# Kernel tuning notes

Measured on AMD Instinct MI355X. Metric: run time of the kernel, lower is better.

## Reference

```python
import jax, jax.numpy as jnp
from jax import lax
import numpy as np


def _conv(x, w):
    # x: [B,Cin,H,W], w: [Cout,Cin,kh,kw] -> [B,Cout,H,W], SAME padding
    return lax.conv_general_dilated(x, w, (1, 1), 'SAME')


def setup_inputs() -> dict:
    key = jax.random.key(0)
    ks = jax.random.split(key, 16)
    B, Hh, W = 8, 256, 256
    inputs = jax.random.normal(ks[0], (B, Hh, W), jnp.float32)
    H0 = jax.random.normal(ks[1], (B, Hh, W), jnp.float32)
    C0 = jax.random.normal(ks[2], (B, 2, Hh, W), jnp.float32)
    # learned scalars: c2 ~ U(0,1), sf ~ N(0, 0.01) shifted away from 0 (it is a divisor)
    c2 = jax.random.uniform(ks[3], (1,), jnp.float32, 0.0, 1.0)
    sf = 0.01 * jax.random.normal(ks[4], (1,), jnp.float32) + 0.02
    # RedNet (assumed small conv encoder-decoder): 1->32->64->32->1, 3x3 SAME, ReLU
    w1 = 0.1 * jax.random.normal(ks[5], (32, 1, 3, 3), jnp.float32)
    b1 = jnp.zeros((32,), jnp.float32)
    w2 = 0.1 * jax.random.normal(ks[6], (64, 32, 3, 3), jnp.float32)
    b2 = jnp.zeros((64,), jnp.float32)
    w3 = 0.1 * jax.random.normal(ks[7], (32, 64, 3, 3), jnp.float32)
    b3 = jnp.zeros((32,), jnp.float32)
    w4 = 0.1 * jax.random.normal(ks[8], (1, 32, 3, 3), jnp.float32)
    b4 = jnp.zeros((1,), jnp.float32)
    return dict(inputs=inputs, H0=H0, C0=C0, c2=c2, sf=sf,
                w1=w1, b1=b1, w2=w2, b2=b2, w3=w3, b3=b3, w4=w4, b4=b4)


def reference(inputs, H0, C0, c2, sf, w1, b1, w2, b2, w3, b3, w4, b4):
    # Fixed 5-point Laplacian stencil (non-trainable in the original module)
    lap_k = jnp.array([[0., 1., 0.], [1., -4., 1.], [0., 1., 0.]],
                      dtype=inputs.dtype)[None, None]  # [1,1,3,3]

    # torch chain: C' = permute/matmul(Wcc^T)/permute + wcu*U
    #   reduces exactly to: C'[:,0] = inputs, C'[:,1] = C_old[:,0]
    C_new = jnp.stack([inputs, C0[:, 0]], axis=1)  # [B,2,H,W]

    V = inputs - H0  # [B,H,W]

    # H = whc . C' = 2*C'[:,0] - C'[:,1] = 2*inputs - C_old[:,0]
    lap = _conv(inputs[:, None], lap_k)[:, 0]  # [B,H,W]
    H = 2.0 * inputs - C0[:, 0] + c2 * lap

    # RedNet on scaled residual V
    h = (V / sf)[:, None]  # [B,1,H,W]
    h = jax.nn.relu(_conv(h, w1) + b1[None, :, None, None])
    h = jax.nn.relu(_conv(h, w2) + b2[None, :, None, None])
    h = jax.nn.relu(_conv(h, w3) + b3[None, :, None, None])
    V_hat = (_conv(h, w4) + b4[None, :, None, None])[:, 0] * sf  # [B,H,W]

    outputs = H + V_hat
    return (outputs, H, C_new, V, V_hat)
```

## Files before the change

### kernel.cpp

```cpp
#include <hip/hip_runtime.h>

#define PLANE 65536
#define WIDTH 256
#define PADW 258
#define PADPLANE 66564

typedef __bf16 v8bf __attribute__((ext_vector_type(8)));
typedef float  v4f  __attribute__((ext_vector_type(4)));

typedef const __attribute__((address_space(1))) unsigned int* gas_ptr;
typedef __attribute__((address_space(3))) unsigned int* las_ptr;

__device__ __forceinline__ void gl_lds(const void* g, void* l) {
  __builtin_amdgcn_global_load_lds((gas_ptr)g, (las_ptr)l, 16, 0, 0);
}

__device__ __forceinline__ int swz(int c) {
  return (c & ~7) | ((c & 7) ^ ((c >> 3) & 7));
}

__device__ __forceinline__ int m6(int x) { return x >= 6 ? x - 6 : x; }

__device__ __forceinline__ unsigned int pack2(float a, float b) {
  __bf16 ba = (__bf16)a, bb = (__bf16)b;
  unsigned short sa = __builtin_bit_cast(unsigned short, ba);
  unsigned short sb = __builtin_bit_cast(unsigned short, bb);
  return (unsigned int)sa | ((unsigned int)sb << 16);
}

#define WT_N 37440
#define ZR_N (8 * 1028 * 32)
__global__ __launch_bounds__(256) void wz_k(
    const float* __restrict__ w1, const float* __restrict__ w2,
    const float* __restrict__ w3, const float* __restrict__ w4,
    float* __restrict__ w1t, __bf16* __restrict__ B2t,
    __bf16* __restrict__ B3t, float* __restrict__ w4t,
    __bf16* __restrict__ a1, __bf16* __restrict__ a3)
{
  int t = blockIdx.x * 256 + threadIdx.x;
  if (t < WT_N) {
    if (t < 288) {
      int tap = t >> 5, cout = t & 31;
      w1t[t] = w1[cout * 9 + tap];
    }
    int t2 = t - 288;
    if (t2 >= 0 && t2 < 18432) {
      int cout = t2 / 288, k = t2 % 288;
      int tap = k / 32, cin = k % 32;
      B2t[t2] = (__bf16)w2[cout * 288 + cin * 9 + tap];
    }
    int t3 = t - (288 + 18432);
    if (t3 >= 0 && t3 < 18432) {
      int cout = t3 / 576, k = t3 % 576;
      int tap = k / 64, cin = k % 64;
      B3t[t3] = (__bf16)w3[cout * 576 + cin * 9 + tap];
    }
    int t4 = t - (288 + 18432 + 18432);
    if (t4 >= 0 && t4 < 288) {
      int tap = t4 >> 5, cin = t4 & 31;
      w4t[t4] = w4[cin * 9 + tap];
    }
    return;
  }
  int idx = t - WT_N;
  if (idx >= ZR_N) return;
  unsigned int* p;
  const int R1 = 8 * 1028 * 16;
  if (idx < R1) p = (unsigned int*)a1;
  else         { p = (unsigned int*)a3; idx -= R1; }
  int ch = idx & 15;
  int pr = idx >> 4;
  int b = pr / 1028, r = pr % 1028;
  int y, x;
  if      (r < 258) { y = 0;           x = r; }
  else if (r < 516) { y = 257;         x = r - 258; }
  else if (r < 772) { y = r - 516 + 1; x = 0; }
  else              { y = r - 772 + 1; x = 257; }
  p[((size_t)b * PADPLANE + y * PADW + x) * 16 + ch] = 0;
}

__global__ __launch_bounds__(256) void prepconv1_k(
    const float* __restrict__ inputs, const float* __restrict__ H0,
    const float* __restrict__ C0, const float* __restrict__ c2p,
    const float* __restrict__ sfp, const float* __restrict__ w1t,
    const float* __restrict__ b1, float* __restrict__ dout,
    __bf16* __restrict__ act1)
{
  const int x = threadIdx.x, y = blockIdx.x, b = blockIdx.y;
  const int p = b * PLANE + y * WIDTH + x;
  const float c2 = c2p[0], sf = sfp[0], rsf = 1.0f / sf;

  float iv[3][3], hv[3][3];
  #pragma unroll
  for (int dy = 0; dy < 3; dy++) {
    int yy = y + dy - 1;
    #pragma unroll
    for (int dx = 0; dx < 3; dx++) {
      int xx = x + dx - 1;
      bool ok = (yy >= 0 && yy < 256 && xx >= 0 && xx < 256);
      int pn = p + (dy - 1) * WIDTH + (dx - 1);
      iv[dy][dx] = ok ? inputs[pn] : 0.f;
      hv[dy][dx] = ok ? H0[pn]     : 0.f;
    }
  }
  const float in = iv[1][1], h0 = hv[1][1];
  const float c0a = C0[b * 131072 + y * WIDTH + x];
  float lap = iv[0][1] + iv[2][1] + iv[1][0] + iv[1][2] - 4.f * in;
  float Hv = 2.f * in - c0a + c2 * lap;
  float V  = in - h0;
  dout[524288 + p]  = Hv;
  dout[2097152 + p] = V;
  dout[1048576 + b * 131072 + y * WIDTH + x]         = in;
  dout[1048576 + b * 131072 + 65536 + y * WIDTH + x] = c0a;

  float acc[32];
  #pragma unroll
  for (int i = 0; i < 32; i++) acc[i] = b1[i];
  #pragma unroll
  for (int tap = 0; tap < 9; tap++) {
    float v = (iv[tap / 3][tap % 3] - hv[tap / 3][tap % 3]) * rsf;
    const float* wp = w1t + tap * 32;
    #pragma unroll
    for (int i = 0; i < 32; i++) acc[i] = fmaf(wp[i], v, acc[i]);
  }
  unsigned int u[16];
  #pragma unroll
  for (int j = 0; j < 16; j++)
    u[j] = pack2(fmaxf(acc[2*j], 0.f), fmaxf(acc[2*j+1], 0.f));
  size_t pa = ((size_t)b * PADPLANE + (y+1) * PADW + (x+1)) * 32;
  uint4* op = reinterpret_cast<uint4*>(act1 + pa);
  #pragma unroll
  for (int j = 0; j < 4; j++)
    op[j] = make_uint4(u[4*j], u[4*j+1], u[4*j+2], u[4*j+3]);
}

#define A1ROWB 4352
#define A2ROWB 8448
__global__ __launch_bounds__(512, 4) void conv23_k(
    const __bf16* __restrict__ act1, const __bf16* __restrict__ B2t,
    const float* __restrict__ b2, const __bf16* __restrict__ B3t,
    const float* __restrict__ b3, __bf16* __restrict__ act3)
{
  const int lane = threadIdx.x & 63, wave = threadIdx.x >> 6;
  const int l15 = lane & 15, q = lane >> 4;
  const int y0 = blockIdx.x * 16, xt = blockIdx.y, b = blockIdx.z;
  const int x0 = xt * 64;
  __shared__ __align__(16) char smem[6 * A2ROWB + 6 * A1ROWB + 1024];
  char* a2r = smem;
  char* a1r = smem + 6 * A2ROWB;
  const __bf16* plane = act1 + (size_t)b * PADPLANE * 32;

  if (wave < 4) {
    auto stageA1 = [&](int k, int slot) {
      int a = y0 - 1 + k;
      a = a < 0 ? 0 : (a > 257 ? 257 : a);
      const char* g = (const char*)(plane + ((size_t)a * PADW + x0 - 1) * 32);
      char* lrow = a1r + slot * A1ROWB;
      const int base = wave * 68;
      gl_lds(g + (size_t)swz(base + lane) * 16, lrow + base * 16);
      if (lane < 4)
        gl_lds(g + (size_t)swz(base + 64 + lane) * 16, lrow + (base + 64) * 16);
    };

    v8bf breg2[9];
    #pragma unroll
    for (int tap = 0; tap < 9; tap++)
      breg2[tap] = *(const v8bf*)(B2t + (size_t)(wave * 16 + l15) * 288
                                      + tap * 32 + q * 8);
    const v4f bv2 = *(const v4f*)(b2 + wave * 16 + q * 4);

    auto zrow = [&](int sl) {
      char* drow = a2r + sl * A2ROWB;
      int c = threadIdx.x;
      *(uint4*)(drow + (size_t)c * 16)         = make_uint4(0,0,0,0);
      *(uint4*)(drow + (size_t)(c + 256) * 16) = make_uint4(0,0,0,0);
      if (c < 16)
        *(uint4*)(drow + (size_t)(c + 512) * 16) = make_uint4(0,0,0,0);
    };

    auto producePair = [&](int t, int s) {
      const int s1 = m6(s + 1);
      const bool z0 = (y0 + t == 0) || (y0 + t == 257);
      const bool z1 = (y0 + t + 1 == 0) || (y0 + t + 1 == 257);
      if (z0) zrow(s);
      if (z1) zrow(s1);
      if (z0 && z1) return;
      v4f acc0[5], acc1v[5];
      #pragma unroll
      for (int m = 0; m < 5; m++) { acc0[m] = bv2; acc1v[m] = bv2; }
      #pragma unroll
      for (int r = 0; r < 4; r++) {
        if (z0 && r == 0) continue;
        if (z1 && r == 3) continue;
        const char* srow = a1r + m6(s + r) * A1ROWB;
        #pragma unroll
        for (int dx = 0; dx < 3; dx++) {
          #pragma unroll
          for (int m = 0; m < 5; m++) {
            int j = m * 16 + l15 + dx;
            v8bf af = *(const v8bf*)(srow + (size_t)swz(j * 4 + q) * 16);
            if (!z0 && r <= 2)
              acc0[m] = __builtin_amdgcn_mfma_f32_16x16x32_bf16(
                  breg2[r * 3 + dx], af, acc0[m], 0, 0, 0);
            if (!z1 && r >= 1)
              acc1v[m] = __builtin_amdgcn_mfma_f32_16x16x32_bf16(
                  breg2[(r - 1) * 3 + dx], af, acc1v[m], 0, 0, 0);
          }
        }
      }
      const int c = wave * 2 + (q >> 1), boff = (q & 1) * 8;
      #pragma unroll
      for (int rr = 0; rr < 2; rr++) {
        if (rr == 0 && z0) continue;
        if (rr == 1 && z1) continue;
        char* drow = a2r + (rr ? s1 : s) * A2ROWB;
        v4f* A = rr ? acc1v : acc0;
        #pragma unroll
        for (int m = 0; m < 5; m++) {
          int px = m * 16 + l15;
          bool w = (m < 4) || (l15 < 2);
          if (x0 == 0   && px == 0)  w = false;
          if (x0 == 192 && px == 65) w = false;
          if (w) {
            unsigned int lo = pack2(fmaxf(A[m][0], 0.f), fmaxf(A[m][1], 0.f));
            unsigned int hi = pack2(fmaxf(A[m][2], 0.f), fmaxf(A[m][3], 0.f));
            *(uint2*)(drow + (size_t)swz(px * 8 + c) * 16 + boff)
                = make_uint2(lo, hi);
          }
        }
        if (x0 == 0 && threadIdx.x < 8)
          *(uint4*)(drow + (size_t)swz(threadIdx.x) * 16) = make_uint4(0,0,0,0);
        if (x0 == 192 && threadIdx.x < 8)
          *(uint4*)(drow + (size_t)swz(520 + threadIdx.x) * 16) = make_uint4(0,0,0,0);
      }
    };

    #pragma unroll
    for (int k = 0; k < 6; k++) stageA1(k, k);
    asm volatile("s_waitcnt vmcnt(0)" ::: "memory");
    __builtin_amdgcn_s_barrier();
    __builtin_amdgcn_sched_barrier(0);
    producePair(0, 0); producePair(2, 2);
    asm volatile("s_waitcnt lgkmcnt(0)" ::: "memory");
    __builtin_amdgcn_s_barrier();
    __builtin_amdgcn_sched_barrier(0);
    stageA1(6, 0); stageA1(7, 1);
    asm volatile("s_waitcnt vmcnt(0)" ::: "memory");
    __builtin_amdgcn_s_barrier();
    __builtin_amdgcn_sched_barrier(0);

    int sb = 2;
    for (int ps = 0; ps < 8; ps++) {
      int r0 = 2 * ps + 8, r1 = 2 * ps + 9;
      stageA1(r0 > 19 ? 19 : r0, sb);
      stageA1(r1 > 19 ? 19 : r1, m6(sb + 1));
      if (2 * ps + 4 <= 17) producePair(2 * ps + 4, m6(sb + 2));
      asm volatile("s_waitcnt vmcnt(0) lgkmcnt(0)" ::: "memory");
      __builtin_amdgcn_s_barrier();
      __builtin_amdgcn_sched_barrier(0);
      sb = m6(sb + 2);
    }
  } else {
    const int cw = wave - 4;
    const int Mh = cw >> 1, ntw = cw & 1;
    v8bf breg3[9][2];
    #pragma unroll
    for (int tap = 0; tap < 9; tap++)
      #pragma unroll
      for (int kb = 0; kb < 2; kb++)
        breg3[tap][kb] = *(const v8bf*)(B3t + (size_t)(ntw * 16 + l15) * 576
                                            + tap * 64 + kb * 32 + q * 8);
    const float bv3 = b3[ntw * 16 + l15];

    __builtin_amdgcn_s_barrier();
    __builtin_amdgcn_s_barrier();
    __builtin_amdgcn_s_barrier();

    int sc = 0;
    for (int ps = 0; ps < 8; ps++) {
      v4f acc3[2][2];
      #pragma unroll
      for (int rr = 0; rr < 2; rr++)
        #pragma unroll
        for (int mt = 0; mt < 2; mt++)
          acc3[rr][mt] = (v4f){bv3, bv3, bv3, bv3};

      __builtin_amdgcn_s_setprio(1);
      #pragma unroll
      for (int t = 0; t < 4; t++) {
        const char* srow = a2r + m6(sc + t) * A2ROWB;
        #pragma unroll
        for (int dx = 0; dx < 3; dx++) {
          #pragma unroll
          for (int kb = 0; kb < 2; kb++) {
            v8bf af[2];
            #pragma unroll
            for (int mt = 0; mt < 2; mt++) {
              int P = Mh * 32 + mt * 16 + l15 + dx;
              af[mt] = *(const v8bf*)(srow + (size_t)swz(P * 8 + kb * 4 + q) * 16);
            }
            #pragma unroll
            for (int mt = 0; mt < 2; mt++) {
              if (t <= 2)
                acc3[0][mt] = __builtin_amdgcn_mfma_f32_16x16x32_bf16(
                    af[mt], breg3[t * 3 + dx][kb], acc3[0][mt], 0, 0, 0);
              if (t >= 1)
                acc3[1][mt] = __builtin_amdgcn_mfma_f32_16x16x32_bf16(
                    af[mt], breg3[(t - 1) * 3 + dx][kb], acc3[1][mt], 0, 0, 0);
            }
          }
        }
      }
      __builtin_amdgcn_s_setprio(0);

      #pragma unroll
      for (int rr = 0; rr < 2; rr++) {
        size_t rb = ((size_t)b * PADPLANE
                     + (size_t)(y0 + 2 * ps + rr + 1) * PADW + x0 + 1) * 32;
        #pragma unroll
        for (int mt = 0; mt < 2; mt++) {
          #pragma unroll
          for (int r = 0; r < 4; r++) {
            int px = Mh * 32 + mt * 16 + q * 4 + r;
            act3[rb + (size_t)px * 32 + ntw * 16 + l15] =
                (__bf16)fmaxf(acc3[rr][mt][r], 0.f);
          }
        }
      }
      __builtin_amdgcn_s_barrier();
      __builtin_amdgcn_sched_barrier(0);
      sc = m6(sc + 2);
    }
  }
}

#define C4ROWB 16512
__global__ __launch_bounds__(256, 2) void conv4_k(
    const __bf16* __restrict__ act3, const float* __restrict__ w4t,
    const float* __restrict__ b4, const float* __restrict__ sfp,
    float* __restrict__ dout)
{
  const int x = threadIdx.x, lane = threadIdx.x & 63, wave = threadIdx.x >> 6;
  const int y0 = blockIdx.x * 2, b = blockIdx.y;
  const float b4v = b4[0], sf = sfp[0];
  const __bf16* plane = act3 + (size_t)b * PADPLANE * 32;
  __shared__ __align__(16) char smem[4 * C4ROWB];

  #pragma unroll
  for (int r = 0; r < 4; r++) {
    const char* g = (const char*)(plane + (size_t)(y0 + r) * PADW * 32);
    char* lrow = smem + r * C4ROWB;
    #pragma unroll
    for (int k = 0; k < 4; k++) {
      int c = k * 256 + wave * 64 + lane;
      gl_lds(g + (size_t)swz(c) * 16, lrow + (k * 256 + wave * 64) * 16);
    }
    if (wave == 0 && lane < 8) {
      int c = 1024 + lane;
      gl_lds(g + (size_t)swz(c) * 16, lrow + 1024 * 16);
    }
  }
  asm volatile("s_waitcnt vmcnt(0)" ::: "memory");
  __builtin_amdgcn_s_barrier();

  float acc0 = b4v, acc1 = b4v;
  #pragma unroll
  for (int t = 0; t < 4; t++) {
    const char* srow = smem + t * C4ROWB;
    uint4 L[12];
    #pragma unroll
    for (int j = 0; j < 12; j++) {
      int chunk = (x + (j >> 2)) * 4 + (j & 3);
      L[j] = *(const uint4*)(srow + (size_t)swz(chunk) * 16);
    }
    #pragma unroll
    for (int j = 0; j < 12; j++) {
      const int dx = j >> 2, c0 = (j & 3) * 8;
      unsigned int uu[4] = {L[j].x, L[j].y, L[j].z, L[j].w};
      float f[8];
      #pragma unroll
      for (int k = 0; k < 4; k++) {
        f[2*k]   = __builtin_bit_cast(float, uu[k] << 16);
        f[2*k+1] = __builtin_bit_cast(float, uu[k] & 0xFFFF0000u);
      }
      if (t <= 2) {
        const float* wp = w4t + (t * 3 + dx) * 32 + c0;
        #pragma unroll
        for (int k = 0; k < 8; k++) acc0 = fmaf(wp[k], f[k], acc0);
      }
      if (t >= 1) {
        const float* wp = w4t + ((t - 1) * 3 + dx) * 32 + c0;
        #pragma unroll
        for (int k = 0; k < 8; k++) acc1 = fmaf(wp[k], f[k], acc1);
      }
    }
  }
  size_t p0 = ((size_t)b << 16) + (size_t)y0 * WIDTH + x;
  float vh0 = acc0 * sf, vh1 = acc1 * sf;
  dout[p0]                   = dout[524288 + p0] + vh0;
  dout[2621440 + p0]         = vh0;
  dout[p0 + WIDTH]           = dout[524288 + p0 + WIDTH] + vh1;
  dout[2621440 + p0 + WIDTH] = vh1;
}

extern "C" void kernel_launch(void* const* d_in, const int* in_sizes, int n_in,
                              void* d_out, int out_size, void* d_ws, size_t ws_size,
                              hipStream_t stream) {
  const float* inputs = (const float*)d_in[0];
  const float* H0     = (const float*)d_in[1];
  const float* C0     = (const float*)d_in[2];
  const float* c2     = (const float*)d_in[3];
  const float* sf     = (const float*)d_in[4];
  const float* w1     = (const float*)d_in[5];
  const float* b1     = (const float*)d_in[6];
  const float* w2     = (const float*)d_in[7];
  const float* b2     = (const float*)d_in[8];
  const float* w3     = (const float*)d_in[9];
  const float* b3     = (const float*)d_in[10];
  const float* w4     = (const float*)d_in[11];
  const float* b4     = (const float*)d_in[12];
  float* out = (float*)d_out;
  float* ws  = (float*)d_ws;

  float*  w1t  = ws;
  float*  w4t  = ws + 288;
  __bf16* B2t  = (__bf16*)(ws + 576);
  __bf16* B3t  = (__bf16*)(ws + 9792);
  __bf16* act1 = (__bf16*)(ws + 19008);
  __bf16* act3 = act1 + (size_t)8 * PADPLANE * 32;

  wz_k<<<1175, 256, 0, stream>>>(w1, w2, w3, w4, w1t, B2t, B3t, w4t,
                                 act1, act3);
  prepconv1_k<<<dim3(256, 8), 256, 0, stream>>>(inputs, H0, C0, c2, sf,
                                                w1t, b1, out, act1);
  conv23_k<<<dim3(16, 4, 8), 512, 0, stream>>>(act1, B2t, b2, B3t, b3, act3);
  conv4_k<<<dim3(128, 8), 256, 0, stream>>>(act3, w4t, b4, sf, out);
}
```

Measured before the change: 163.3 us.

## Swap MFMA operands for packed conv3 stores and retile conv4 blocks

In conv3, the MFMA A/B operands are swapped so each lane holds four consecutive output channels for one pixel. The ReLU outputs can then be packed into a single 8-byte bf16 store instead of four scattered 2-byte stores, and the bias is loaded as a vector to match. conv4 is retiled so each block covers four rows by 128 columns instead of two rows by 256. This cuts redundant halo-row loads per output row and changes the grid shape. The trade-offs are more LDS rows per block and a different block count, which may affect occupancy.

```diff
diff --git a/kernel.cpp b/kernel.cpp
--- a/kernel.cpp
+++ b/kernel.cpp
@@ -270,7 +270,7 @@
       for (int kb = 0; kb < 2; kb++)
         breg3[tap][kb] = *(const v8bf*)(B3t + (size_t)(ntw * 16 + l15) * 576
                                             + tap * 64 + kb * 32 + q * 8);
-    const float bv3 = b3[ntw * 16 + l15];
+    const v4f bv3 = *(const v4f*)(b3 + ntw * 16 + q * 4);
 
     __builtin_amdgcn_s_barrier();
     __builtin_amdgcn_s_barrier();
@@ -283,7 +283,7 @@
       for (int rr = 0; rr < 2; rr++)
         #pragma unroll
         for (int mt = 0; mt < 2; mt++)
-          acc3[rr][mt] = (v4f){bv3, bv3, bv3, bv3};
+          acc3[rr][mt] = bv3;
 
       __builtin_amdgcn_s_setprio(1);
       #pragma unroll
@@ -303,10 +303,10 @@
             for (int mt = 0; mt < 2; mt++) {
               if (t <= 2)
                 acc3[0][mt] = __builtin_amdgcn_mfma_f32_16x16x32_bf16(
-                    af[mt], breg3[t * 3 + dx][kb], acc3[0][mt], 0, 0, 0);
+                    breg3[t * 3 + dx][kb], af[mt], acc3[0][mt], 0, 0, 0);
               if (t >= 1)
                 acc3[1][mt] = __builtin_amdgcn_mfma_f32_16x16x32_bf16(
-                    af[mt], breg3[(t - 1) * 3 + dx][kb], acc3[1][mt], 0, 0, 0);
+                    breg3[(t - 1) * 3 + dx][kb], af[mt], acc3[1][mt], 0, 0, 0);
             }
           }
         }
@@ -319,12 +319,13 @@
                      + (size_t)(y0 + 2 * ps + rr + 1) * PADW + x0 + 1) * 32;
         #pragma unroll
         for (int mt = 0; mt < 2; mt++) {
-          #pragma unroll
-          for (int r = 0; r < 4; r++) {
-            int px = Mh * 32 + mt * 16 + q * 4 + r;
-            act3[rb + (size_t)px * 32 + ntw * 16 + l15] =
-                (__bf16)fmaxf(acc3[rr][mt][r], 0.f);
-          }
+          int px = Mh * 32 + mt * 16 + l15;
+          unsigned int lo = pack2(fmaxf(acc3[rr][mt][0], 0.f),
+                                  fmaxf(acc3[rr][mt][1], 0.f));
+          unsigned int hi = pack2(fmaxf(acc3[rr][mt][2], 0.f),
+                                  fmaxf(acc3[rr][mt][3], 0.f));
+          *(uint2*)(act3 + rb + (size_t)px * 32 + ntw * 16 + q * 4)
+              = make_uint2(lo, hi);
         }
       }
       __builtin_amdgcn_s_barrier();
@@ -334,43 +335,46 @@
   }
 }
 
-#define C4ROWB 16512
+#define C4ROWB 8320
 __global__ __launch_bounds__(256, 2) void conv4_k(
     const __bf16* __restrict__ act3, const float* __restrict__ w4t,
     const float* __restrict__ b4, const float* __restrict__ sfp,
     float* __restrict__ dout)
 {
-  const int x = threadIdx.x, lane = threadIdx.x & 63, wave = threadIdx.x >> 6;
-  const int y0 = blockIdx.x * 2, b = blockIdx.y;
+  const int tid = threadIdx.x, lane = tid & 63, wave = tid >> 6;
+  const int y0 = blockIdx.x * 4, xh = blockIdx.y, b = blockIdx.z;
+  const int xbase = xh * 128;
   const float b4v = b4[0], sf = sfp[0];
   const __bf16* plane = act3 + (size_t)b * PADPLANE * 32;
-  __shared__ __align__(16) char smem[4 * C4ROWB];
-
-  #pragma unroll
-  for (int r = 0; r < 4; r++) {
-    const char* g = (const char*)(plane + (size_t)(y0 + r) * PADW * 32);
+  __shared__ __align__(16) char smem[6 * C4ROWB];
+
+  #pragma unroll
+  for (int r = 0; r < 6; r++) {
+    const char* g = (const char*)(plane + ((size_t)(y0 + r) * PADW + xbase) * 32);
     char* lrow = smem + r * C4ROWB;
-    #pragma unroll
-    for (int k = 0; k < 4; k++) {
-      int c = k * 256 + wave * 64 + lane;
-      gl_lds(g + (size_t)swz(c) * 16, lrow + (k * 256 + wave * 64) * 16);
-    }
-    if (wave == 0 && lane < 8) {
-      int c = 1024 + lane;
-      gl_lds(g + (size_t)swz(c) * 16, lrow + 1024 * 16);
+    const int base = wave * 130;
+    #pragma unroll
+    for (int j = 0; j < 2; j++) {
+      int c = base + j * 64 + lane;
+      gl_lds(g + (size_t)swz(c) * 16, lrow + (base + j * 64) * 16);
+    }
+    if (lane < 2) {
+      int c = base + 128 + lane;
+      gl_lds(g + (size_t)swz(c) * 16, lrow + (base + 128) * 16);
     }
   }
   asm volatile("s_waitcnt vmcnt(0)" ::: "memory");
   __builtin_amdgcn_s_barrier();
 
+  const int px = tid & 127, pp = tid >> 7;
   float acc0 = b4v, acc1 = b4v;
   #pragma unroll
   for (int t = 0; t < 4; t++) {
-    const char* srow = smem + t * C4ROWB;
+    const char* srow = smem + (2 * pp + t) * C4ROWB;
     uint4 L[12];
     #pragma unroll
     for (int j = 0; j < 12; j++) {
-      int chunk = (x + (j >> 2)) * 4 + (j & 3);
+      int chunk = (px + (j >> 2)) * 4 + (j & 3);
       L[j] = *(const uint4*)(srow + (size_t)swz(chunk) * 16);
     }
     #pragma unroll
@@ -395,7 +399,7 @@
       }
     }
   }
-  size_t p0 = ((size_t)b << 16) + (size_t)y0 * WIDTH + x;
+  size_t p0 = ((size_t)b << 16) + (size_t)(y0 + 2 * pp) * WIDTH + xbase + px;
   float vh0 = acc0 * sf, vh1 = acc1 * sf;
   dout[p0]                   = dout[524288 + p0] + vh0;
   dout[2621440 + p0]         = vh0;
@@ -434,5 +438,5 @@
   prepconv1_k<<<dim3(256, 8), 256, 0, stream>>>(inputs, H0, C0, c2, sf,
                                                 w1t, b1, out, act1);
   conv23_k<<<dim3(16, 4, 8), 512, 0, stream>>>(act1, B2t, b2, B3t, b3, act3);
-  conv4_k<<<dim3(128, 8), 256, 0, stream>>>(act3, w4t, b4, sf, out);
-}
+  conv4_k<<<dim3(64, 2, 8), 256, 0, stream>>>(act3, w4t, b4, sf, out);
+}
```

Result: no change. 162.7 us (median of 2 runs) (-0.3%).
